# Kernel optimization log

Measured on AMD Instinct MI355X. Metric: run time of the kernel, lower is better.

## Reference

```python
import jax, jax.numpy as jnp
import numpy as np
from jax import lax

B, N, S, K, C, OUT = 8, 4096, 1024, 24, 64, 128
IN = 2 * C + 3  # 131: grouped(C+3) concat anchor feature(C)
EPS_BN = 1e-5


def _bn_params(key, c):
    k1, k2, k3, k4 = jax.random.split(key, 4)
    gamma = jax.random.uniform(k1, (c,), minval=0.5, maxval=1.5)
    beta = jax.random.normal(k2, (c,)) * 0.1
    mean = jax.random.normal(k3, (c,)) * 0.1
    var = jax.random.uniform(k4, (c,), minval=0.5, maxval=1.5)
    return jnp.stack([gamma, beta, mean, var])  # [4,c]


def setup_inputs() -> dict:
    key = jax.random.key(0)
    ks = jax.random.split(key, 20)
    w = lambda k, shp: jax.random.normal(k, shp) * 0.05
    inp = {
        "xyz": jax.random.normal(ks[0], (B, N, 3)),
        "points": jax.random.normal(ks[1], (B, N, C)),
        "affine_alpha": jnp.ones((1, 1, 1, C + 3)),
        "affine_beta": jnp.zeros((1, 1, 1, C + 3)),
        "transfer_w": w(ks[2], (OUT, IN)),
        "transfer_b": jnp.zeros((OUT,)),
        "transfer_bn": _bn_params(ks[3], OUT),
        "pre_w1": w(ks[4], (2, OUT, OUT)),
        "pre_b1": jnp.zeros((2, OUT)),
        "pre_bn1": jnp.stack([_bn_params(ks[5], OUT), _bn_params(ks[6], OUT)]),
        "pre_w2": w(ks[7], (2, OUT, OUT)),
        "pre_b2": jnp.zeros((2, OUT)),
        "pre_bn2": jnp.stack([_bn_params(ks[8], OUT), _bn_params(ks[9], OUT)]),
        "pos_w1": w(ks[10], (2, OUT, OUT)),
        "pos_b1": jnp.zeros((2, OUT)),
        "pos_bn1": jnp.stack([_bn_params(ks[11], OUT), _bn_params(ks[12], OUT)]),
        "pos_w2": w(ks[13], (2, OUT, OUT)),
        "pos_b2": jnp.zeros((2, OUT)),
        "pos_bn2": jnp.stack([_bn_params(ks[14], OUT), _bn_params(ks[15], OUT)]),
    }
    return inp


def _gather(x, idx):
    # x: [B,N,D], idx: [B,...] -> [B,...,D]
    return jax.vmap(lambda a, i: a[i])(x, idx)


def _sqdist(a, b):
    # a: [B,S,3], b: [B,N,3] -> [B,S,N]
    return (jnp.sum(a * a, -1)[:, :, None] + jnp.sum(b * b, -1)[:, None, :]
            - 2.0 * jnp.einsum('bsd,bnd->bsn', a, b))


def _fps(xyz, s):
    # furthest point sampling, starts at index 0 (matches CUDA pointnet2 impl)
    b, n, _ = xyz.shape
    def step(carry, _):
        dist, last = carry
        p = jnp.take_along_axis(xyz, last[:, None, None], axis=1)  # [B,1,3]
        d = jnp.sum((xyz - p) ** 2, -1)
        dist = jnp.minimum(dist, d)
        nxt = jnp.argmax(dist, axis=-1).astype(jnp.int32)
        return (dist, nxt), nxt
    init = (jnp.full((b, n), 1e10, xyz.dtype), jnp.zeros((b,), jnp.int32))
    _, idxs = lax.scan(step, init, None, length=s - 1)  # [S-1,B]
    return jnp.concatenate([jnp.zeros((1, b), jnp.int32), idxs], 0).T  # [B,S]


def _conv_bn(x, w, b, bn, act=True):
    # 1x1 Conv1d + BatchNorm (eval mode) + optional ReLU. x: [M,Cin,L]
    y = jnp.einsum('oc,mcl->mol', w, x) + b[None, :, None]
    g, be, mu, var = bn[0], bn[1], bn[2], bn[3]
    y = (y - mu[None, :, None]) * (g[None, :, None] / jnp.sqrt(var[None, :, None] + EPS_BN)) + be[None, :, None]
    return jax.nn.relu(y) if act else y


def _res_block(x, w1, b1, bn1, w2, b2, bn2):
    y = _conv_bn(x, w1, b1, bn1, act=True)
    y = _conv_bn(y, w2, b2, bn2, act=False)
    return jax.nn.relu(y + x)


def reference(xyz, points, affine_alpha, affine_beta,
              transfer_w, transfer_b, transfer_bn,
              pre_w1, pre_b1, pre_bn1, pre_w2, pre_b2, pre_bn2,
              pos_w1, pos_b1, pos_bn1, pos_w2, pos_b2, pos_bn2):
    b, n, _ = xyz.shape
    # ---- LocalGrouper ----
    fps_idx = _fps(xyz, S)                      # [B,S]
    new_xyz = _gather(xyz, fps_idx)             # [B,S,3]
    new_points = _gather(points, fps_idx)       # [B,S,C]
    d = _sqdist(new_xyz, xyz)                   # [B,S,N]
    _, idx = lax.top_k(-d, K)                   # k nearest -> [B,S,K]
    grouped_xyz = _gather(xyz, idx)             # [B,S,K,3]
    grouped_points = _gather(points, idx)       # [B,S,K,C]
    grouped = jnp.concatenate([grouped_points, grouped_xyz], -1)  # [B,S,K,C+3]
    # anchor normalize
    mean = jnp.concatenate([new_points, new_xyz], -1)[:, :, None, :]
    diff = grouped - mean
    std = jnp.std(diff.reshape(b, -1), axis=-1, ddof=1)[:, None, None, None]
    grouped = affine_alpha * (diff / (std + 1e-5)) + affine_beta
    anchor = jnp.broadcast_to(new_points[:, :, None, :], (b, S, K, C))
    feats = jnp.concatenate([grouped, anchor], -1)  # [B,S,K,2C+3]
    # ---- PreExtraction ----
    x = feats.transpose(0, 1, 3, 2).reshape(b * S, IN, K)  # [B*S,131,K]
    x = _conv_bn(x, transfer_w, transfer_b, transfer_bn, act=True)
    for i in range(2):
        x = _res_block(x, pre_w1[i], pre_b1[i], pre_bn1[i], pre_w2[i], pre_b2[i], pre_bn2[i])
    x = jnp.max(x, axis=-1)                     # adaptive max pool over K
    x = x.reshape(b, S, OUT).transpose(0, 2, 1)  # [B,OUT,S]
    # ---- PosExtraction ----
    for i in range(2):
        x = _res_block(x, pos_w1[i], pos_b1[i], pos_bn1[i], pos_w2[i], pos_b2[i], pos_bn2[i])
    return x  # [B,128,1024]
```

## Files before the change

kernel.cpp:

```cpp
#include <hip/hip_runtime.h>
#include <hip/hip_bf16.h>
#include <stdint.h>
#include <math.h>

#define DEVINL static __device__ __forceinline__

static constexpr int BB = 8, NN = 4096, SS = 1024, KK = 24, CC = 64;
static constexpr int INCH = 131, OUTCH = 128;

typedef __attribute__((ext_vector_type(8))) short short8v;
typedef __attribute__((ext_vector_type(4))) float f32x4;

#define MFMA16(a, b, c) __builtin_amdgcn_mfma_f32_16x16x32_bf16(a, b, c, 0, 0, 0)

DEVINL unsigned short f2bf(float v) {
  __hip_bfloat16 h = __float2bfloat16(v);
  return *reinterpret_cast<unsigned short*>(&h);
}
DEVINL float bfbits2f(unsigned short u) {
  unsigned x = ((unsigned)u) << 16;
  return __int_as_float(x);
}

__global__ __launch_bounds__(256) void k_prep_xyz(
    const float* __restrict__ xyz,
    float* __restrict__ xs, float* __restrict__ ys,
    float* __restrict__ zs, float* __restrict__ sb) {
  int e = blockIdx.x * 256 + threadIdx.x;
  if (e >= BB * NN) return;
  float x = xyz[e * 3 + 0];
  float y = xyz[e * 3 + 1];
  float z = xyz[e * 3 + 2];
  xs[e] = x; ys[e] = y; zs[e] = z;
  sb[e] = __fadd_rn(__fadd_rn(__fmul_rn(x, x), __fmul_rn(y, y)), __fmul_rn(z, z));
}

__global__ __launch_bounds__(256) void k_prep_w(
    const float* __restrict__ tw,
    const float* __restrict__ pw1, const float* __restrict__ pw2,
    const float* __restrict__ qw1, const float* __restrict__ qw2,
    const float* __restrict__ tb,  const float* __restrict__ tbn,
    const float* __restrict__ pb1, const float* __restrict__ pbn1,
    const float* __restrict__ pb2, const float* __restrict__ pbn2,
    const float* __restrict__ qb1, const float* __restrict__ qbn1,
    const float* __restrict__ qb2, const float* __restrict__ qbn2,
    float* __restrict__ wt_sq, float* __restrict__ bnsb,
    unsigned short* __restrict__ wfhi, unsigned short* __restrict__ wflo) {
  int e = blockIdx.x * 256 + threadIdx.x;
  const int NSQ = 8 * 128 * 128;
  const int NBN = 9 * 128;
  const int NFR = 168 * 64;
  if (e < NSQ) {
    int layer = e >> 14, m = e & 16383;
    int ci = m >> 7, co = m & 127;
    const float* src;
    switch (layer) {
      case 0: src = pw1;         break;
      case 1: src = pw2;         break;
      case 2: src = pw1 + 16384; break;
      case 3: src = pw2 + 16384; break;
      case 4: src = qw1;         break;
      case 5: src = qw2;         break;
      case 6: src = qw1 + 16384; break;
      default: src = qw2 + 16384; break;
    }
    wt_sq[layer * 16384 + ci * 128 + co] = src[co * 128 + ci];
  } else if (e < NSQ + NBN) {
    int r = e - NSQ;
    int L = r >> 7, co = r & 127;
    const float *bn, *bc;
    switch (L) {
      case 0: bn = tbn;        bc = tb;        break;
      case 1: bn = pbn1;       bc = pb1;       break;
      case 2: bn = pbn2;       bc = pb2;       break;
      case 3: bn = pbn1 + 512; bc = pb1 + 128; break;
      case 4: bn = pbn2 + 512; bc = pb2 + 128; break;
      case 5: bn = qbn1;       bc = qb1;       break;
      case 6: bn = qbn2;       bc = qb2;       break;
      case 7: bn = qbn1 + 512; bc = qb1 + 128; break;
      default: bn = qbn2 + 512; bc = qb2 + 128; break;
    }
    float g  = bn[co];
    float be = bn[128 + co];
    float mu = bn[256 + co];
    float va = bn[384 + co];
    float bcv = bc[co];
    float sc = g / sqrtf(va + 1e-5f);
    float bi = (bcv - mu) * sc + be;
    bnsb[L * 256 + co] = sc;
    bnsb[L * 256 + 128 + co] = bi;
  } else if (e < NSQ + NBN + NFR) {
    int r = e - (NSQ + NBN);
    int T = r >> 6, lane = r & 63;
    int L, ks, mt;
    if (T < 40) { L = 0; ks = T >> 3; mt = T & 7; }
    else { int r2 = T - 40; L = 1 + (r2 >> 5); int r3 = r2 & 31; ks = r3 >> 3; mt = r3 & 7; }
    const float* src;
    int K, stride;
    switch (L) {
      case 0:  src = tw;          K = 131; stride = 131; break;
      case 1:  src = pw1;         K = 128; stride = 128; break;
      case 2:  src = pw2;         K = 128; stride = 128; break;
      case 3:  src = pw1 + 16384; K = 128; stride = 128; break;
      default: src = pw2 + 16384; K = 128; stride = 128; break;
    }
    int m = lane & 15, kb = lane >> 4;
    int co = mt * 16 + m;
    int base = (T * 64 + lane) * 8;
#pragma unroll
    for (int j = 0; j < 8; j++) {
      int ci = ks * 32 + kb * 8 + j;
      float w = (ci < K) ? src[co * stride + ci] : 0.f;
      unsigned short h = f2bf(w);
      unsigned short l = f2bf(w - bfbits2f(h));
      wfhi[base + j] = h;
      wflo[base + j] = l;
    }
  }
}

DEVINL float wave_max_f32_l63(float x) {
#define STEPF(C)                                                                \
  {                                                                             \
    int o = __builtin_amdgcn_update_dpp(0xff800000, __float_as_int(x), C, 0xf, 0xf, false); \
    x = fmaxf(x, __int_as_float(o));                                            \
  }
  STEPF(0x111) STEPF(0x112) STEPF(0x114) STEPF(0x118) STEPF(0x142) STEPF(0x143)
#undef STEPF
  return x;
}

__global__ __launch_bounds__(256, 1) void k_fps(
    const float* __restrict__ xs, const float* __restrict__ ys,
    const float* __restrict__ zs, const float* __restrict__ sb,
    const float* __restrict__ points,
    float* __restrict__ nxyz, float* __restrict__ sa, float* __restrict__ newp) {
  __shared__ float lxl[NN], lyl[NN], lzl[NN];
  __shared__ unsigned long long pk[2][4];
  __shared__ int fpsl[SS];
  const int b = blockIdx.x, t = threadIdx.x;
  const int wid = t >> 6, lane = t & 63;
  const float* bx = xs + b * NN;
  const float* by = ys + b * NN;
  const float* bz = zs + b * NN;
  float rx[16], ry[16], rz[16], d[16];
  const int n0 = t * 16;
#pragma unroll
  for (int j = 0; j < 16; j++) {
    rx[j] = bx[n0 + j]; ry[j] = by[n0 + j]; rz[j] = bz[n0 + j];
    lxl[n0 + j] = rx[j]; lyl[n0 + j] = ry[j]; lzl[n0 + j] = rz[j];
    d[j] = 1e10f;
  }
  __syncthreads();
  float px = lxl[0], py = lyl[0], pz = lzl[0];
  if (t == 0) fpsl[0] = 0;
#pragma unroll 1
  for (int i = 1; i < SS; i++) {
    float bestval = -1.f;
    int bestn = 0;
#pragma unroll
    for (int j = 0; j < 16; j++) {
      float dx = __fsub_rn(rx[j], px);
      float dy = __fsub_rn(ry[j], py);
      float dz = __fsub_rn(rz[j], pz);
      float dd = __fadd_rn(__fadd_rn(__fmul_rn(dx, dx), __fmul_rn(dy, dy)),
                           __fmul_rn(dz, dz));
      float nd = fminf(d[j], dd);
      d[j] = nd;
      if (nd > bestval) { bestval = nd; bestn = n0 + j; }
    }
    float wmax = __int_as_float(
        __builtin_amdgcn_readlane(__float_as_int(wave_max_f32_l63(bestval)), 63));
    unsigned long long el = __ballot(bestval == wmax);
    int fl = (int)__ffsll(el) - 1;
    int wn = __builtin_amdgcn_readlane(bestn, fl);
    if (lane == 0)
      pk[i & 1][wid] = ((unsigned long long)__float_as_uint(wmax) << 32) |
                       (unsigned)(NN - 1 - wn);
    __syncthreads();
    const unsigned long long* P = pk[i & 1];
    unsigned long long k0 = P[0], k1 = P[1], k2 = P[2], k3 = P[3];
    unsigned long long m01 = k1 > k0 ? k1 : k0;
    unsigned long long m23 = k3 > k2 ? k3 : k2;
    unsigned long long g = m23 > m01 ? m23 : m01;
    int n = NN - 1 - (int)(unsigned)g;
    px = lxl[n]; py = lyl[n]; pz = lzl[n];
    if (t == 0) fpsl[i] = n;
  }
  __syncthreads();
  for (int s = t; s < SS; s += 256) {
    int row = fpsl[s];
    nxyz[(b * SS + s) * 3 + 0] = lxl[row];
    nxyz[(b * SS + s) * 3 + 1] = lyl[row];
    nxyz[(b * SS + s) * 3 + 2] = lzl[row];
    sa[b * SS + s] = sb[b * NN + row];
  }
  for (int e = t; e < SS * CC; e += 256) {
    int s = e >> 6, c = e & 63;
    int row = fpsl[s];
    newp[(b * SS + s) * CC + c] = points[(b * NN + row) * CC + c];
  }
}

__global__ __launch_bounds__(256, 2) void k_knn(
    const float* __restrict__ xs, const float* __restrict__ ys,
    const float* __restrict__ zs,
    const float* __restrict__ nxyz, const float* __restrict__ sa,
    const float* __restrict__ points, const float* __restrict__ newp,
    int* __restrict__ knn, double* __restrict__ spart) {
  __shared__ float lx[NN], ly[NN], lz[NN];
  __shared__ int selk[4][KK];
  const int blk = blockIdx.x, t = threadIdx.x, wid = t >> 6, lane = t & 63;
  const int b = blk >> 8;
  for (int e = t; e < NN; e += 256) {
    lx[e] = xs[b * NN + e]; ly[e] = ys[b * NN + e]; lz[e] = zs[b * NN + e];
  }
  __syncthreads();
  const int q = blk * 4 + wid;
  float qx = nxyz[q * 3 + 0], qy = nxyz[q * 3 + 1], qz = nxyz[q * 3 + 2];
  float qa = sa[q];
  unsigned keys[64];
#pragma unroll
  for (int j = 0; j < 64; j++) {
    int n = j * 64 + lane;
    float x = lx[n], y = ly[n], z = lz[n];
    float sbn = __fadd_rn(__fadd_rn(__fmul_rn(x, x), __fmul_rn(y, y)), __fmul_rn(z, z));
    float dot = __fadd_rn(__fadd_rn(__fmul_rn(qx, x), __fmul_rn(qy, y)), __fmul_rn(qz, z));
    float dd = __fsub_rn(__fadd_rn(qa, sbn), __fmul_rn(2.0f, dot));
    unsigned u = __float_as_uint(dd);
    u ^= (0x80000000u | (unsigned)((int)u >> 31));
    keys[j] = u;
  }
#pragma unroll 1
  for (int r = 0; r < KK; r++) {
    unsigned bv = keys[0];
    int bj = 0;
#pragma unroll
    for (int j = 1; j < 64; j++) {
      if (keys[j] < bv) { bv = keys[j]; bj = j; }
    }
    unsigned long long gk = ((unsigned long long)bv << 32) | (unsigned)(bj * 64 + lane);
#pragma unroll
    for (int m = 1; m < 64; m <<= 1) {
      unsigned long long o = __shfl_xor(gk, m);
      gk = o < gk ? o : gk;
    }
    int n = (int)(unsigned)gk;
    if (lane == 0) { knn[q * KK + r] = n; selk[wid][r] = n; }
    if (lane == (n & 63)) {
      int jj = n >> 6;
#pragma unroll
      for (int j = 0; j < 64; j++)
        if (j == jj) keys[j] = 0xFFFFFFFFu;
    }
  }
  double s1 = 0.0, s2 = 0.0;
#pragma unroll 1
  for (int i = 0; i < 26; i++) {
    int e = lane + 64 * i;
    if (e < KK * 67) {
      int k = e / 67, c = e - k * 67;
      int n = selk[wid][k];
      float g, mm;
      if (c < CC) {
        g = points[(b * NN + n) * CC + c];
        mm = newp[q * CC + c];
      } else {
        int cc = c - CC;
        g = cc == 0 ? lx[n] : (cc == 1 ? ly[n] : lz[n]);
        mm = nxyz[q * 3 + cc];
      }
      float v = __fsub_rn(g, mm);
      s1 += (double)v;
      s2 += (double)v * (double)v;
    }
  }
#pragma unroll
  for (int m = 1; m < 64; m <<= 1) {
    s1 += __shfl_xor(s1, m);
    s2 += __shfl_xor(s2, m);
  }
  if (lane == 0) { spart[q * 2 + 0] = s1; spart[q * 2 + 1] = s2; }
}

__global__ __launch_bounds__(256) void k_stdfin(
    const double* __restrict__ spart, float* __restrict__ stdp) {
  __shared__ double a1[256], a2[256];
  const int b = blockIdx.x, t = threadIdx.x;
  double s1 = 0.0, s2 = 0.0;
  for (int i = t; i < SS; i += 256) {
    s1 += spart[(b * SS + i) * 2 + 0];
    s2 += spart[(b * SS + i) * 2 + 1];
  }
  a1[t] = s1; a2[t] = s2;
  __syncthreads();
  for (int w = 128; w > 0; w >>= 1) {
    if (t < w) { a1[t] += a1[t + w]; a2[t] += a2[t + w]; }
    __syncthreads();
  }
  if (t == 0) {
    const double n = (double)SS * KK * 67;
    double m = a1[0] / n;
    double var = (a2[0] - a1[0] * m) / (n - 1.0);
    if (var < 0.0) var = 0.0;
    float stdf = (float)sqrt(var);
    stdp[b] = stdf + 1e-5f;
  }
}

static constexpr int BST = 168;
static constexpr int XST = 132;

__global__ __launch_bounds__(256, 3) void k_pre(
    const float* __restrict__ points,
    const float* __restrict__ alpha, const float* __restrict__ beta,
    const float* __restrict__ xs, const float* __restrict__ ys, const float* __restrict__ zs,
    const float* __restrict__ nxyz, const float* __restrict__ newp,
    const float* __restrict__ stdp, const int* __restrict__ knn,
    const unsigned short* __restrict__ wfhi, const unsigned short* __restrict__ wflo,
    const float* __restrict__ bnsb, float* __restrict__ pre_out) {
  __shared__ unsigned short Bhi[32 * BST];
  __shared__ unsigned short Blo[32 * BST];
  __shared__ float Xres[32 * XST];
  __shared__ int kn[KK];
  __shared__ float npl[CC], nxl[3], al[67], bt[67];
  __shared__ float stds;
  const int q = blockIdx.x, b = q >> 10, t = threadIdx.x;
  for (int e = t; e < 32 * BST; e += 256) { Bhi[e] = 0; Blo[e] = 0; }
  if (t < KK) kn[t] = knn[q * KK + t];
  if (t < 67) { al[t] = alpha[t]; bt[t] = beta[t]; }
  if (t < CC) npl[t] = newp[q * CC + t];
  if (t < 3) nxl[t] = nxyz[q * 3 + t];
  if (t == 0) stds = stdp[b];
  __syncthreads();
  for (int e = t; e < KK * 67; e += 256) {
    int k = e / 67, c = e - k * 67;
    int n = kn[k];
    float g, mm;
    if (c < CC) {
      g = points[(b * NN + n) * CC + c];
      mm = npl[c];
    } else {
      int cc = c - CC;
      g = cc == 0 ? xs[b * NN + n] : (cc == 1 ? ys[b * NN + n] : zs[b * NN + n]);
      mm = nxl[cc];
    }
    float v = __fsub_rn(g, mm);
    float tt = __fdiv_rn(v, stds);
    float val = __fadd_rn(__fmul_rn(al[c], tt), bt[c]);
    unsigned short h = f2bf(val);
    Bhi[k * BST + c] = h;
    Blo[k * BST + c] = f2bf(val - bfbits2f(h));
  }
  for (int e = t; e < CC * KK; e += 256) {
    int c = e / KK, k = e - c * KK;
    float val = npl[c];
    unsigned short h = f2bf(val);
    Bhi[k * BST + 67 + c] = h;
    Blo[k * BST + 67 + c] = f2bf(val - bfbits2f(h));
  }
  __syncthreads();

  const int wv = t >> 6, lane = t & 63;
  const int g4 = lane >> 4;
  const int l15 = lane & 15;
  const int mt0 = wv * 2;

#pragma unroll 1
  for (int L = 0; L < 5; ++L) {
    const int nks = (L == 0) ? 5 : 4;
    const int wtb = (L == 0) ? 0 : (8 + 32 * L);
    const bool addres = (L == 2) || (L == 4);
    const bool wres = (L == 0) || (L == 2);
    const bool pool = (L == 4);
    f32x4 acc00 = {0.f, 0.f, 0.f, 0.f}, acc01 = {0.f, 0.f, 0.f, 0.f};
    f32x4 acc10 = {0.f, 0.f, 0.f, 0.f}, acc11 = {0.f, 0.f, 0.f, 0.f};
#pragma unroll 1
    for (int ks = 0; ks < nks; ++ks) {
      const int tb = (wtb + ks * 8 + mt0) * 64 + lane;
      short8v wh0 = *(const short8v*)(wfhi + tb * 8);
      short8v wh1 = *(const short8v*)(wfhi + (tb + 64) * 8);
      short8v wl0 = *(const short8v*)(wflo + tb * 8);
      short8v wl1 = *(const short8v*)(wflo + (tb + 64) * 8);
      const int bo = l15 * BST + ks * 32 + g4 * 8;
      short8v bh0 = *(const short8v*)&Bhi[bo];
      short8v bh1 = *(const short8v*)&Bhi[bo + 16 * BST];
      short8v bl0 = *(const short8v*)&Blo[bo];
      short8v bl1 = *(const short8v*)&Blo[bo + 16 * BST];
      acc00 = MFMA16(wh0, bh0, acc00);
      acc00 = MFMA16(wl0, bh0, acc00);
      acc00 = MFMA16(wh0, bl0, acc00);
      acc01 = MFMA16(wh0, bh1, acc01);
      acc01 = MFMA16(wl0, bh1, acc01);
      acc01 = MFMA16(wh0, bl1, acc01);
      acc10 = MFMA16(wh1, bh0, acc10);
      acc10 = MFMA16(wl1, bh0, acc10);
      acc10 = MFMA16(wh1, bl0, acc10);
      acc11 = MFMA16(wh1, bh1, acc11);
      acc11 = MFMA16(wl1, bh1, acc11);
      acc11 = MFMA16(wh1, bl1, acc11);
    }
    __syncthreads();
    float mx0[4] = {0.f, 0.f, 0.f, 0.f};
    float mx1[4] = {0.f, 0.f, 0.f, 0.f};
    auto ep = [&](const f32x4& a, int mt_i, int nt, float* mxr) {
      const int co0 = (mt0 + mt_i) * 16 + g4 * 4;
      const int kp = nt * 16 + l15;
      const bool valid = kp < KK;
      f32x4 scv = *(const f32x4*)(bnsb + L * 256 + co0);
      f32x4 biv = *(const f32x4*)(bnsb + L * 256 + 128 + co0);
      float y[4];
#pragma unroll
      for (int r = 0; r < 4; r++) y[r] = fmaf(a[r], scv[r], biv[r]);
      if (addres && valid) {
        f32x4 xr = *(const f32x4*)&Xres[kp * XST + co0];
#pragma unroll
        for (int r = 0; r < 4; r++) y[r] += xr[r];
      }
#pragma unroll
      for (int r = 0; r < 4; r++) y[r] = fmaxf(y[r], 0.f);
      if (wres && valid) {
        f32x4 o = {y[0], y[1], y[2], y[3]};
        *(f32x4*)&Xres[kp * XST + co0] = o;
      }
      if (!pool) {
        if (valid) {
          unsigned h01 = (unsigned)f2bf(y[0]) | ((unsigned)f2bf(y[1]) << 16);
          unsigned h23 = (unsigned)f2bf(y[2]) | ((unsigned)f2bf(y[3]) << 16);
          *(uint2*)&Bhi[kp * BST + co0] = make_uint2(h01, h23);
          unsigned l01 = (unsigned)f2bf(y[0] - bfbits2f((unsigned short)(h01 & 0xffff))) |
                         ((unsigned)f2bf(y[1] - bfbits2f((unsigned short)(h01 >> 16))) << 16);
          unsigned l23 = (unsigned)f2bf(y[2] - bfbits2f((unsigned short)(h23 & 0xffff))) |
                         ((unsigned)f2bf(y[3] - bfbits2f((unsigned short)(h23 >> 16))) << 16);
          *(uint2*)&Blo[kp * BST + co0] = make_uint2(l01, l23);
        }
      } else {
#pragma unroll
        for (int r = 0; r < 4; r++) {
          float v = valid ? y[r] : 0.f;
          mxr[r] = fmaxf(mxr[r], v);
        }
      }
    };
    ep(acc00, 0, 0, mx0);
    ep(acc01, 0, 1, mx0);
    ep(acc10, 1, 0, mx1);
    ep(acc11, 1, 1, mx1);
    if (!pool) {
      __syncthreads();
    } else {
#pragma unroll
      for (int dstep = 1; dstep < 16; dstep <<= 1) {
#pragma unroll
        for (int r = 0; r < 4; r++) {
          mx0[r] = fmaxf(mx0[r], __shfl_xor(mx0[r], dstep));
          mx1[r] = fmaxf(mx1[r], __shfl_xor(mx1[r], dstep));
        }
      }
      if (l15 == 0) {
        f32x4 o0 = {mx0[0], mx0[1], mx0[2], mx0[3]};
        f32x4 o1 = {mx1[0], mx1[1], mx1[2], mx1[3]};
        *(f32x4*)&pre_out[q * 128 + mt0 * 16 + g4 * 4] = o0;
        *(f32x4*)&pre_out[q * 128 + (mt0 + 1) * 16 + g4 * 4] = o1;
      }
    }
  }
}

__global__ __launch_bounds__(256, 2) void k_pos(
    const float* __restrict__ pre_out, const float* __restrict__ wt_sq,
    const float* __restrict__ bnsb, float* __restrict__ out) {
  __shared__ float X[128][68];
  __shared__ float Y[128][68];
  const int blk = blockIdx.x, t = threadIdx.x;
  const int b = blk >> 4, s0 = (blk & 15) << 6;
  for (int e = t; e < 128 * 64; e += 256) {
    int sl = e >> 7, c = e & 127;
    X[c][sl] = pre_out[(b * SS + s0 + sl) * 128 + c];
  }
  __syncthreads();
  const int co0 = (t >> 3) << 2, p0 = (t & 7) << 3;
  float acc[4][8];
  auto conv = [&](const float (*IN)[68], const float* wt) {
#pragma unroll
    for (int i = 0; i < 4; i++)
#pragma unroll
      for (int j = 0; j < 8; j++) acc[i][j] = 0.f;
#pragma unroll 2
    for (int ci = 0; ci < 128; ci++) {
      float4 w = *(const float4*)(wt + ci * 128 + co0);
      float4 r0 = *(const float4*)&IN[ci][p0];
      float4 r1 = *(const float4*)&IN[ci][p0 + 4];
      float a[8] = {r0.x, r0.y, r0.z, r0.w, r1.x, r1.y, r1.z, r1.w};
#pragma unroll
      for (int j = 0; j < 8; j++) {
        acc[0][j] = fmaf(w.x, a[j], acc[0][j]);
        acc[1][j] = fmaf(w.y, a[j], acc[1][j]);
        acc[2][j] = fmaf(w.z, a[j], acc[2][j]);
        acc[3][j] = fmaf(w.w, a[j], acc[3][j]);
      }
    }
  };
  conv(X, wt_sq + 4 * 16384);
  {
    const float* bn = bnsb + 5 * 256;
#pragma unroll
    for (int i = 0; i < 4; i++) {
      float sc = bn[co0 + i], bi = bn[128 + co0 + i];
#pragma unroll
      for (int j = 0; j < 8; j++)
        Y[co0 + i][p0 + j] = fmaxf(fmaf(acc[i][j], sc, bi), 0.f);
    }
  }
  __syncthreads();
  conv(Y, wt_sq + 5 * 16384);
  {
    const float* bn = bnsb + 6 * 256;
#pragma unroll
    for (int i = 0; i < 4; i++) {
      float sc = bn[co0 + i], bi = bn[128 + co0 + i];
#pragma unroll
      for (int j = 0; j < 8; j++)
        X[co0 + i][p0 + j] =
            fmaxf(fmaf(acc[i][j], sc, bi) + X[co0 + i][p0 + j], 0.f);
    }
  }
  __syncthreads();
  conv(X, wt_sq + 6 * 16384);
  {
    const float* bn = bnsb + 7 * 256;
#pragma unroll
    for (int i = 0; i < 4; i++) {
      float sc = bn[co0 + i], bi = bn[128 + co0 + i];
#pragma unroll
      for (int j = 0; j < 8; j++)
        Y[co0 + i][p0 + j] = fmaxf(fmaf(acc[i][j], sc, bi), 0.f);
    }
  }
  __syncthreads();
  conv(Y, wt_sq + 7 * 16384);
  {
    const float* bn = bnsb + 8 * 256;
#pragma unroll
    for (int i = 0; i < 4; i++) {
      float sc = bn[co0 + i], bi = bn[128 + co0 + i];
      float4 o0, o1;
      float v;
      v = fmaxf(fmaf(acc[i][0], sc, bi) + X[co0 + i][p0 + 0], 0.f); o0.x = v;
      v = fmaxf(fmaf(acc[i][1], sc, bi) + X[co0 + i][p0 + 1], 0.f); o0.y = v;
      v = fmaxf(fmaf(acc[i][2], sc, bi) + X[co0 + i][p0 + 2], 0.f); o0.z = v;
      v = fmaxf(fmaf(acc[i][3], sc, bi) + X[co0 + i][p0 + 3], 0.f); o0.w = v;
      v = fmaxf(fmaf(acc[i][4], sc, bi) + X[co0 + i][p0 + 4], 0.f); o1.x = v;
      v = fmaxf(fmaf(acc[i][5], sc, bi) + X[co0 + i][p0 + 5], 0.f); o1.y = v;
      v = fmaxf(fmaf(acc[i][6], sc, bi) + X[co0 + i][p0 + 6], 0.f); o1.z = v;
      v = fmaxf(fmaf(acc[i][7], sc, bi) + X[co0 + i][p0 + 7], 0.f); o1.w = v;
      float* op = &out[(size_t)(b * 128 + co0 + i) * SS + s0 + p0];
      *(float4*)op = o0;
      *(float4*)(op + 4) = o1;
    }
  }
}

extern "C" void kernel_launch(void* const* d_in, const int* in_sizes, int n_in,
                              void* d_out, int out_size, void* d_ws, size_t ws_size,
                              hipStream_t stream) {
  (void)in_sizes; (void)n_in; (void)out_size; (void)ws_size;
  const float* xyz    = (const float*)d_in[0];
  const float* points = (const float*)d_in[1];
  const float* alpha  = (const float*)d_in[2];
  const float* beta   = (const float*)d_in[3];
  const float* tw     = (const float*)d_in[4];
  const float* tb     = (const float*)d_in[5];
  const float* tbn    = (const float*)d_in[6];
  const float* pw1    = (const float*)d_in[7];
  const float* pb1    = (const float*)d_in[8];
  const float* pbn1   = (const float*)d_in[9];
  const float* pw2    = (const float*)d_in[10];
  const float* pb2    = (const float*)d_in[11];
  const float* pbn2   = (const float*)d_in[12];
  const float* qw1    = (const float*)d_in[13];
  const float* qb1    = (const float*)d_in[14];
  const float* qbn1   = (const float*)d_in[15];
  const float* qw2    = (const float*)d_in[16];
  const float* qb2    = (const float*)d_in[17];
  const float* qbn2   = (const float*)d_in[18];

  char* ws = (char*)d_ws;
  size_t off = 0;
  auto alloc = [&](size_t bytes) -> char* {
    char* p = ws + off;
    off += (bytes + 255) & ~(size_t)255;
    return p;
  };
  float*  xs    = (float*)alloc(BB * NN * 4);
  float*  ys    = (float*)alloc(BB * NN * 4);
  float*  zs    = (float*)alloc(BB * NN * 4);
  float*  sb    = (float*)alloc(BB * NN * 4);
  float*  wt_sq = (float*)alloc(8 * 16384 * 4);
  float*  bnsb  = (float*)alloc(9 * 256 * 4);
  unsigned short* wfhi = (unsigned short*)alloc(168 * 512 * 2);
  unsigned short* wflo = (unsigned short*)alloc(168 * 512 * 2);
  float*  nxyz  = (float*)alloc(BB * SS * 3 * 4);
  float*  sa    = (float*)alloc(BB * SS * 4);
  float*  newp  = (float*)alloc(BB * SS * CC * 4);
  int*    knn   = (int*)alloc(BB * SS * KK * 4);
  double* spart = (double*)alloc(BB * SS * 2 * 8);
  float*  stdp  = (float*)alloc(256);
  float*  preo  = (float*)alloc((size_t)BB * SS * 128 * 4);
  float*  out   = (float*)d_out;

  const int prep_n = 8 * 128 * 128 + 9 * 128 + 168 * 64;
  hipLaunchKernelGGL(k_prep_xyz, dim3((BB * NN + 255) / 256), dim3(256), 0, stream,
                     xyz, xs, ys, zs, sb);
  hipLaunchKernelGGL(k_prep_w, dim3((prep_n + 255) / 256), dim3(256), 0, stream,
                     tw, pw1, pw2, qw1, qw2, tb, tbn, pb1, pbn1, pb2, pbn2,
                     qb1, qbn1, qb2, qbn2, wt_sq, bnsb, wfhi, wflo);
  hipLaunchKernelGGL(k_fps, dim3(BB), dim3(256), 0, stream,
                     xs, ys, zs, sb, points, nxyz, sa, newp);
  hipLaunchKernelGGL(k_knn, dim3(BB * SS / 4), dim3(256), 0, stream,
                     xs, ys, zs, nxyz, sa, points, newp, knn, spart);
  hipLaunchKernelGGL(k_stdfin, dim3(BB), dim3(256), 0, stream, spart, stdp);
  hipLaunchKernelGGL(k_pre, dim3(BB * SS), dim3(256), 0, stream,
                     points, alpha, beta, xs, ys, zs, nxyz, newp, stdp, knn,
                     wfhi, wflo, bnsb, preo);
  hipLaunchKernelGGL(k_pos, dim3(BB * SS / 64), dim3(256), 0, stream,
                     preo, wt_sq, bnsb, out);
}
```

Measured before the change: 1.063 ms.

## Pack two batches per FPS block and tree-reduce per-thread argmax

The furthest point sampling kernel now processes two batch items in one 512-thread block, each half holding its own shared copy of the coordinates and its own partial-max slots. The goal is to put more independent waves on each compute unit, so the latency of the serial 1023-step loop is better hidden. The per-thread 16-element argmax becomes a pairwise tree instead of a sequential compare chain, which shortens the dependency path in each iteration. The trade-off is that both halves now share each __syncthreads, so they are coupled, and shared memory per block doubles. A local variable in k_pre is also renamed to avoid shadowing the new h.

```diff
diff --git a/kernel.cpp b/kernel.cpp
--- a/kernel.cpp
+++ b/kernel.cpp
@@ -130,34 +130,35 @@
   return x;
 }
 
-__global__ __launch_bounds__(256, 1) void k_fps(
+__global__ __launch_bounds__(512, 1) void k_fps(
     const float* __restrict__ xs, const float* __restrict__ ys,
     const float* __restrict__ zs, const float* __restrict__ sb,
     const float* __restrict__ points,
     float* __restrict__ nxyz, float* __restrict__ sa, float* __restrict__ newp) {
-  __shared__ float lxl[NN], lyl[NN], lzl[NN];
-  __shared__ unsigned long long pk[2][4];
-  __shared__ int fpsl[SS];
-  const int b = blockIdx.x, t = threadIdx.x;
-  const int wid = t >> 6, lane = t & 63;
-  const float* bx = xs + b * NN;
-  const float* by = ys + b * NN;
-  const float* bz = zs + b * NN;
+  __shared__ float lxl[2][NN], lyl[2][NN], lzl[2][NN];
+  __shared__ unsigned long long pk[2][2][4];
+  __shared__ int fpsl[2][SS];
+  const int t = threadIdx.x;
+  const int h = t >> 8;
+  const int tl = t & 255;
+  const int bb = blockIdx.x * 2 + h;
+  const int wl = tl >> 6, lane = t & 63;
+  const float* bx = xs + bb * NN;
+  const float* by = ys + bb * NN;
+  const float* bz = zs + bb * NN;
   float rx[16], ry[16], rz[16], d[16];
-  const int n0 = t * 16;
+  const int n0 = tl * 16;
 #pragma unroll
   for (int j = 0; j < 16; j++) {
     rx[j] = bx[n0 + j]; ry[j] = by[n0 + j]; rz[j] = bz[n0 + j];
-    lxl[n0 + j] = rx[j]; lyl[n0 + j] = ry[j]; lzl[n0 + j] = rz[j];
+    lxl[h][n0 + j] = rx[j]; lyl[h][n0 + j] = ry[j]; lzl[h][n0 + j] = rz[j];
     d[j] = 1e10f;
   }
   __syncthreads();
-  float px = lxl[0], py = lyl[0], pz = lzl[0];
-  if (t == 0) fpsl[0] = 0;
+  float px = lxl[h][0], py = lyl[h][0], pz = lzl[h][0];
+  if (tl == 0) fpsl[h][0] = 0;
 #pragma unroll 1
   for (int i = 1; i < SS; i++) {
-    float bestval = -1.f;
-    int bestn = 0;
 #pragma unroll
     for (int j = 0; j < 16; j++) {
       float dx = __fsub_rn(rx[j], px);
@@ -165,40 +166,62 @@
       float dz = __fsub_rn(rz[j], pz);
       float dd = __fadd_rn(__fadd_rn(__fmul_rn(dx, dx), __fmul_rn(dy, dy)),
                            __fmul_rn(dz, dz));
-      float nd = fminf(d[j], dd);
-      d[j] = nd;
-      if (nd > bestval) { bestval = nd; bestn = n0 + j; }
-    }
+      d[j] = fminf(d[j], dd);
+    }
+    float v8[8]; int i8[8];
+#pragma unroll
+    for (int j = 0; j < 8; j++) {
+      bool c = d[2 * j] >= d[2 * j + 1];
+      v8[j] = c ? d[2 * j] : d[2 * j + 1];
+      i8[j] = c ? (2 * j) : (2 * j + 1);
+    }
+    float v4[4]; int i4[4];
+#pragma unroll
+    for (int j = 0; j < 4; j++) {
+      bool c = v8[2 * j] >= v8[2 * j + 1];
+      v4[j] = c ? v8[2 * j] : v8[2 * j + 1];
+      i4[j] = c ? i8[2 * j] : i8[2 * j + 1];
+    }
+    float v2[2]; int i2[2];
+#pragma unroll
+    for (int j = 0; j < 2; j++) {
+      bool c = v4[2 * j] >= v4[2 * j + 1];
+      v2[j] = c ? v4[2 * j] : v4[2 * j + 1];
+      i2[j] = c ? i4[2 * j] : i4[2 * j + 1];
+    }
+    bool c0 = v2[0] >= v2[1];
+    float bestval = c0 ? v2[0] : v2[1];
+    int bestn = n0 + (c0 ? i2[0] : i2[1]);
     float wmax = __int_as_float(
         __builtin_amdgcn_readlane(__float_as_int(wave_max_f32_l63(bestval)), 63));
     unsigned long long el = __ballot(bestval == wmax);
     int fl = (int)__ffsll(el) - 1;
     int wn = __builtin_amdgcn_readlane(bestn, fl);
     if (lane == 0)
-      pk[i & 1][wid] = ((unsigned long long)__float_as_uint(wmax) << 32) |
-                       (unsigned)(NN - 1 - wn);
+      pk[i & 1][h][wl] = ((unsigned long long)__float_as_uint(wmax) << 32) |
+                         (unsigned)(NN - 1 - wn);
     __syncthreads();
-    const unsigned long long* P = pk[i & 1];
+    const unsigned long long* P = pk[i & 1][h];
     unsigned long long k0 = P[0], k1 = P[1], k2 = P[2], k3 = P[3];
     unsigned long long m01 = k1 > k0 ? k1 : k0;
     unsigned long long m23 = k3 > k2 ? k3 : k2;
     unsigned long long g = m23 > m01 ? m23 : m01;
     int n = NN - 1 - (int)(unsigned)g;
-    px = lxl[n]; py = lyl[n]; pz = lzl[n];
-    if (t == 0) fpsl[i] = n;
-  }
-  __syncthreads();
-  for (int s = t; s < SS; s += 256) {
-    int row = fpsl[s];
-    nxyz[(b * SS + s) * 3 + 0] = lxl[row];
-    nxyz[(b * SS + s) * 3 + 1] = lyl[row];
-    nxyz[(b * SS + s) * 3 + 2] = lzl[row];
-    sa[b * SS + s] = sb[b * NN + row];
-  }
-  for (int e = t; e < SS * CC; e += 256) {
+    px = lxl[h][n]; py = lyl[h][n]; pz = lzl[h][n];
+    if (tl == 0) fpsl[h][i] = n;
+  }
+  __syncthreads();
+  for (int s = tl; s < SS; s += 256) {
+    int row = fpsl[h][s];
+    nxyz[(bb * SS + s) * 3 + 0] = lxl[h][row];
+    nxyz[(bb * SS + s) * 3 + 1] = lyl[h][row];
+    nxyz[(bb * SS + s) * 3 + 2] = lzl[h][row];
+    sa[bb * SS + s] = sb[bb * NN + row];
+  }
+  for (int e = tl; e < SS * CC; e += 256) {
     int s = e >> 6, c = e & 63;
-    int row = fpsl[s];
-    newp[(b * SS + s) * CC + c] = points[(b * NN + row) * CC + c];
+    int row = fpsl[h][s];
+    newp[(bb * SS + s) * CC + c] = points[(bb * NN + row) * CC + c];
   }
 }
 
@@ -348,16 +371,16 @@
     float v = __fsub_rn(g, mm);
     float tt = __fdiv_rn(v, stds);
     float val = __fadd_rn(__fmul_rn(al[c], tt), bt[c]);
-    unsigned short h = f2bf(val);
-    Bhi[k * BST + c] = h;
-    Blo[k * BST + c] = f2bf(val - bfbits2f(h));
+    unsigned short hh = f2bf(val);
+    Bhi[k * BST + c] = hh;
+    Blo[k * BST + c] = f2bf(val - bfbits2f(hh));
   }
   for (int e = t; e < CC * KK; e += 256) {
     int c = e / KK, k = e - c * KK;
     float val = npl[c];
-    unsigned short h = f2bf(val);
-    Bhi[k * BST + 67 + c] = h;
-    Blo[k * BST + 67 + c] = f2bf(val - bfbits2f(h));
+    unsigned short hh = f2bf(val);
+    Bhi[k * BST + 67 + c] = hh;
+    Blo[k * BST + 67 + c] = f2bf(val - bfbits2f(hh));
   }
   __syncthreads();
 
@@ -615,7 +638,7 @@
   hipLaunchKernelGGL(k_prep_w, dim3((prep_n + 255) / 256), dim3(256), 0, stream,
                      tw, pw1, pw2, qw1, qw2, tb, tbn, pb1, pbn1, pb2, pbn2,
                      qb1, qbn1, qb2, qbn2, wt_sq, bnsb, wfhi, wflo);
-  hipLaunchKernelGGL(k_fps, dim3(BB), dim3(256), 0, stream,
+  hipLaunchKernelGGL(k_fps, dim3(BB / 2), dim3(512), 0, stream,
                      xs, ys, zs, sb, points, nxyz, sa, newp);
   hipLaunchKernelGGL(k_knn, dim3(BB * SS / 4), dim3(256), 0, stream,
                      xs, ys, zs, nxyz, sa, points, newp, knn, spart);
```

Result: slower. 1.521 ms (+43.1%).
